# Kernel optimization log

Measured on AMD Instinct MI355X. Metric: run time of the kernel, lower is better.

The kernel has to match this reference:

```python
import jax, jax.numpy as jnp
import numpy as np

L, N, E, H, R = 2048, 4, 768, 12, 16
ALPHA = 16.0
LORA_SCALE = ALPHA / R
HEAD_DIM = E // H


def setup_inputs() -> dict:
    rng = jax.random.key(0)
    ks = jax.random.split(rng, 15)
    g = lambda i, shape, s=1.0: jax.random.normal(ks[i], shape, jnp.float32) * s
    return {
        "query": g(0, (L, N, E)),
        "key": g(1, (L, N, E)),
        "value": g(2, (L, N, E)),
        "in_proj_weight": g(3, (3 * E, E), 0.02),
        "in_proj_bias": g(4, (3 * E,), 0.02),
        "q_down": g(5, (R, E), 0.02),
        "q_up": g(6, (E, R), 0.02),
        "k_down": g(7, (R, E), 0.02),
        "k_up": g(8, (E, R), 0.02),
        "v_down": g(9, (R, E), 0.02),
        "v_up": g(10, (E, R), 0.02),
        "out_proj_weight": g(11, (E, E), 0.02),
        "out_proj_bias": g(12, (E,), 0.02),
        "out_down": g(13, (R, E), 0.02),
        "out_up": g(14, (E, R), 0.02),
    }


def _lora_linear(x, W, b, down, up):
    # y = x W^T + b + scale * (x down^T) up^T   (LoRA-adapted nn.Linear)
    return x @ W.T + b + LORA_SCALE * ((x @ down.T) @ up.T)


def reference(query, key, value, in_proj_weight, in_proj_bias,
              q_down, q_up, k_down, k_up, v_down, v_up,
              out_proj_weight, out_proj_bias, out_down, out_up):
    Wq, Wk, Wv = jnp.split(in_proj_weight, 3, axis=0)
    bq, bk, bv = jnp.split(in_proj_bias, 3)
    q = _lora_linear(query, Wq, bq, q_down, q_up)   # (L,N,E)
    k = _lora_linear(key, Wk, bk, k_down, k_up)     # (S,N,E)
    v = _lora_linear(value, Wv, bv, v_down, v_up)

    def to_heads(t):  # (T,N,E) -> (N,H,T,hd)
        return t.reshape(t.shape[0], N, H, HEAD_DIM).transpose(1, 2, 0, 3)

    qh, kh, vh = to_heads(q), to_heads(k), to_heads(v)
    scale = 1.0 / jnp.sqrt(jnp.float32(HEAD_DIM))
    scores = jnp.einsum('nhld,nhsd->nhls', qh * scale, kh)  # (N,H,L,S)
    attn = jax.nn.softmax(scores, axis=-1)
    o = jnp.einsum('nhls,nhsd->nhld', attn, vh)             # (N,H,L,hd)
    o = o.transpose(2, 0, 1, 3).reshape(L, N, E)            # (L,N,E)
    return _lora_linear(o, out_proj_weight, out_proj_bias, out_down, out_up)
```

## Files before the change

kernel.cpp:

```cpp
#include <hip/hip_runtime.h>

#define LL 2048
#define NN 4
#define EE 768
#define HH 12
#define RR 16
#define HD 64
#define TT (LL*NN)
#define F3 (3*EE)
#define KA 832

typedef __bf16 bf16;
typedef bf16 bf16x4 __attribute__((ext_vector_type(4)));
typedef bf16 bf16x8 __attribute__((ext_vector_type(8)));
typedef float floatx4 __attribute__((ext_vector_type(4)));
typedef float floatx16 __attribute__((ext_vector_type(16)));
typedef unsigned uintx4 __attribute__((ext_vector_type(4)));

#define ZERO16 (floatx16){0.f,0.f,0.f,0.f,0.f,0.f,0.f,0.f,0.f,0.f,0.f,0.f,0.f,0.f,0.f,0.f}

__global__ __launch_bounds__(256) void cast_x(
    const float* __restrict__ q, const float* __restrict__ k,
    const float* __restrict__ v, bf16* __restrict__ Xa)
{
    const int bid = blockIdx.x;
    const int third = bid / (TT/8);
    const int r0 = (bid % (TT/8)) * 8;
    const float* x = (third == 0) ? q : (third == 1) ? k : v;
    const int tid = threadIdx.x;
    #pragma unroll
    for (int i = 0; i < 6; ++i) {
        const int e4 = i*256 + tid;
        const int row = e4 / 192;
        const int col = (e4 % 192) * 4;
        const float4 f = *(const float4*)(x + (size_t)(r0+row)*EE + col);
        bf16x4 h = { (bf16)f.x, (bf16)f.y, (bf16)f.z, (bf16)f.w };
        *(bf16x4*)(Xa + ((size_t)third*TT + r0 + row)*KA + col) = h;
    }
}

__global__ __launch_bounds__(256) void prep_w(
    const float* __restrict__ W,  const float* __restrict__ qu,
    const float* __restrict__ ku, const float* __restrict__ vu,
    const float* __restrict__ Wo, const float* __restrict__ ou,
    const float* __restrict__ qd, const float* __restrict__ kd,
    const float* __restrict__ vd, const float* __restrict__ odw,
    bf16* __restrict__ Wa, bf16* __restrict__ Dm)
{
    const int f = blockIdx.x;
    const int tid = threadIdx.x;
    if (f < 3072) {
        const float* src;
        const float* up;
        if (f < F3) {
            const int third = f / EE, fe = f % EE;
            src = W + (size_t)f*EE;
            up  = ((third == 0) ? qu : (third == 1) ? ku : vu) + fe*RR;
        } else {
            const int fe = f - F3;
            src = Wo + (size_t)fe*EE;
            up  = ou + fe*RR;
        }
        bf16* row = Wa + (size_t)f*KA;
        #pragma unroll
        for (int i = 0; i < 3; ++i)
            row[i*256 + tid] = (bf16)src[i*256 + tid];
        if (tid < 64)
            row[EE + tid] = (tid < RR) ? (bf16)up[tid] : (bf16)0.f;
    } else {
        const int f2 = f - 3072;
        const int which = f2 >> 4, r = f2 & 15;
        const float* dsrc = (which == 0) ? qd : (which == 1) ? kd
                          : (which == 2) ? vd : odw;
        bf16* drow = Dm + (size_t)f2*EE;
        #pragma unroll
        for (int i = 0; i < 3; ++i)
            drow[i*256 + tid] = (bf16)dsrc[(size_t)r*EE + i*256 + tid];
    }
}

template<int XA>
__global__ __launch_bounds__(256) void lora_rank16(
    bf16* __restrict__ A, const bf16* __restrict__ Dm)
{
    __shared__ float red[4][64][16];
    const int row0 = blockIdx.x * 64;
    const int dn = XA ? (row0 >> 13) : 3;
    const bf16* D = Dm + (size_t)dn*16*EE;
    const int tid = threadIdx.x;
    const int wave = tid >> 6, lane = tid & 63;
    const int quad = lane >> 4, l16 = lane & 15;

    floatx4 acc[4];
    #pragma unroll
    for (int rt = 0; rt < 4; ++rt) acc[rt] = (floatx4){0.f,0.f,0.f,0.f};

    #pragma unroll
    for (int ks = 0; ks < 6; ++ks) {
        const int k0 = wave*192 + ks*32;
        const bf16x8 b = *(const bf16x8*)(D + (size_t)l16*EE + k0 + quad*8);
        #pragma unroll
        for (int rt = 0; rt < 4; ++rt) {
            const bf16x8 a = *(const bf16x8*)(
                A + (size_t)(row0 + rt*16 + l16)*KA + k0 + quad*8);
            acc[rt] = __builtin_amdgcn_mfma_f32_16x16x32_bf16(a, b, acc[rt], 0, 0, 0);
        }
    }

    #pragma unroll
    for (int rt = 0; rt < 4; ++rt)
        #pragma unroll
        for (int rr = 0; rr < 4; ++rr)
            red[wave][rt*16 + quad*4 + rr][l16] = acc[rt][rr];
    __syncthreads();

    {
        const int row = tid >> 2, cq = (tid & 3) * 4;
        bf16x4 o;
        #pragma unroll
        for (int j = 0; j < 4; ++j) {
            const float s = red[0][row][cq+j] + red[1][row][cq+j]
                          + red[2][row][cq+j] + red[3][row][cq+j];
            o[j] = (bf16)s;
        }
        *(bf16x4*)(A + (size_t)(row0+row)*KA + EE + cq) = o;
    }
    #pragma unroll
    for (int p = 0; p < 3; ++p) {
        const int id = p*256 + tid;
        const int row = id / 12, c = id % 12;
        *(bf16x4*)(A + (size_t)(row0+row)*KA + 784 + c*4) = (bf16x4){};
    }
}

template<int MODE>
__global__ __launch_bounds__(256) void gemm_aug(
    const bf16* __restrict__ A,
    const bf16* __restrict__ B,
    const float* __restrict__ bias,
    bf16* __restrict__ qo, bf16* __restrict__ ko, bf16* __restrict__ vo,
    float* __restrict__ fo)
{
    __shared__ bf16 As[128][72];
    __shared__ bf16 Bs[128][72];
    const int t0 = blockIdx.x * 128;
    const int f0 = blockIdx.y * 128;
    const int tid = threadIdx.x;
    const int wave = tid >> 6, lane = tid & 63;
    const int quad = lane >> 4, l16 = lane & 15;
    const int m0 = (wave & 1) * 64;
    const int n0 = (wave >> 1) * 64;

    const int third = (MODE == 0) ? (f0 / EE) : 0;
    const bf16* Aeff = (MODE == 0) ? (A + (size_t)third*TT*KA) : A;

    floatx4 acc[4][4];
    #pragma unroll
    for (int rt = 0; rt < 4; ++rt)
        #pragma unroll
        for (int ct = 0; ct < 4; ++ct) acc[rt][ct] = (floatx4){0.f,0.f,0.f,0.f};

    for (int kb = 0; kb < KA/64; ++kb) {
        __syncthreads();
        #pragma unroll
        for (int c = 0; c < 4; ++c) {
            int id = c*256 + tid;
            int row = id >> 3, cg = id & 7;
            *(bf16x8*)(&As[row][cg*8]) =
                *(const bf16x8*)(Aeff + (size_t)(t0+row)*KA + kb*64 + cg*8);
            *(bf16x8*)(&Bs[row][cg*8]) =
                *(const bf16x8*)(B + (size_t)(f0+row)*KA + kb*64 + cg*8);
        }
        __syncthreads();
        #pragma unroll
        for (int kc = 0; kc < 2; ++kc) {
            bf16x8 a[4], bfr[4];
            #pragma unroll
            for (int rt = 0; rt < 4; ++rt)
                a[rt] = *(const bf16x8*)(&As[m0 + rt*16 + l16][kc*32 + quad*8]);
            #pragma unroll
            for (int ct = 0; ct < 4; ++ct)
                bfr[ct] = *(const bf16x8*)(&Bs[n0 + ct*16 + l16][kc*32 + quad*8]);
            #pragma unroll
            for (int rt = 0; rt < 4; ++rt)
                #pragma unroll
                for (int ct = 0; ct < 4; ++ct)
                    acc[rt][ct] = __builtin_amdgcn_mfma_f32_16x16x32_bf16(
                        a[rt], bfr[ct], acc[rt][ct], 0, 0, 0);
        }
    }

    #pragma unroll
    for (int rt = 0; rt < 4; ++rt) {
        #pragma unroll
        for (int r = 0; r < 4; ++r) {
            const int t = t0 + m0 + rt*16 + quad*4 + r;
            #pragma unroll
            for (int ct = 0; ct < 4; ++ct) {
                const int fl = n0 + ct*16 + l16;
                float c = acc[rt][ct][r] + bias[f0 + fl];
                if (MODE == 0) {
                    const int fe = (f0 % EE) + fl;
                    const int h = fe >> 6, d = fe & 63;
                    const int l = t >> 2, n = t & 3;
                    const size_t idx = (((size_t)(n*HH + h)*LL) + l)*HD + d;
                    if (third == 0)      qo[idx] = (bf16)(c * 0.180336877f);
                    else if (third == 1) ko[idx] = (bf16)c;
                    else                 vo[idx] = (bf16)c;
                } else {
                    fo[(size_t)t*EE + f0 + fl] = c;
                }
            }
        }
    }
}

__global__ __launch_bounds__(256) void vtrans(
    const bf16* __restrict__ vin, bf16* __restrict__ vout)
{
    __shared__ bf16 T[64][64];
    const int nh = blockIdx.x >> 5;
    const int l0 = (blockIdx.x & 31) * 64;
    const int tid = threadIdx.x;
    const bf16* src = vin + ((size_t)nh*LL + l0)*HD;
    #pragma unroll
    for (int c = 0; c < 2; ++c) {
        int id = c*256 + tid;
        int row = id >> 3, dg = id & 7;
        int pg = dg ^ (row & 7);
        *(bf16x8*)(&T[row][pg*8]) = *(const bf16x8*)(src + row*HD + dg*8);
    }
    __syncthreads();
    bf16* dst = vout + (size_t)nh*HD*LL;
    const int wave = tid >> 6, lane = tid & 63;
    #pragma unroll
    for (int it = 0; it < 2; ++it) {
        const int d  = it*32 + wave*8 + (lane >> 3);
        const int cg = lane & 7;
        bf16x8 vv;
        #pragma unroll
        for (int j = 0; j < 8; ++j) {
            const int lrow = cg*8 + j;
            const int pg = (d >> 3) ^ (lrow & 7);
            vv[j] = T[lrow][pg*8 + (d & 7)];
        }
        *(bf16x8*)(dst + (size_t)d*LL + l0 + cg*8) = vv;
    }
}

__device__ __forceinline__ unsigned pk_bf16(float a, float b) {
    unsigned r;
    asm("v_cvt_pk_bf16_f32 %0, %1, %2" : "=v"(r) : "v"(a), "v"(b));
    return r;
}

__device__ __forceinline__ void compute_tile(
    const bf16 (&KS)[64][64], const bf16 (&VS)[64][64],
    const bf16x8 (&bq)[4], const bf16x8& ones, const floatx16& z16,
    int l32, int hi, int sw,
    floatx16& oacc0, floatx16& oacc1, floatx16& oaccS)
{
    #pragma unroll
    for (int ss = 0; ss < 2; ++ss) {
        bf16x8 ak[4];
        #pragma unroll
        for (int t4 = 0; t4 < 4; ++t4)
            ak[t4] = *(const bf16x8*)(&KS[ss*32 + l32][((t4*2 + hi) ^ sw) * 8]);

        __builtin_amdgcn_s_setprio(1);
        floatx16 sacc = __builtin_amdgcn_mfma_f32_32x32x16_bf16(
            ak[0], bq[0], z16, 0, 0, 0);
        #pragma unroll
        for (int t4 = 1; t4 < 4; ++t4)
            sacc = __builtin_amdgcn_mfma_f32_32x32x16_bf16(
                ak[t4], bq[t4], sacc, 0, 0, 0);
        __builtin_amdgcn_s_setprio(0);

        bf16x8 bv[4];
        #pragma unroll
        for (int tl = 0; tl < 2; ++tl)
            #pragma unroll
            for (int dt = 0; dt < 2; ++dt)
                bv[tl*2 + dt] = *(const bf16x8*)(
                    &VS[dt*32 + l32][((ss*4 + tl*2 + hi) ^ sw) * 8]);

        float p[16];
        #pragma unroll
        for (int r = 0; r < 16; ++r) p[r] = __builtin_amdgcn_exp2f(sacc[r]);

        union { uintx4 u; bf16x8 h; } fr0, fr1;
        {
            unsigned c0 = pk_bf16(p[0], p[1]);
            unsigned c1 = pk_bf16(p[2], p[3]);
            unsigned c2 = pk_bf16(p[4], p[5]);
            unsigned c3 = pk_bf16(p[6], p[7]);
            asm("v_permlane32_swap_b32 %0, %1" : "+v"(c0), "+v"(c2));
            asm("v_permlane32_swap_b32 %0, %1" : "+v"(c1), "+v"(c3));
            fr0.u = (uintx4){c0, c1, c2, c3};
        }
        {
            unsigned c0 = pk_bf16(p[8],  p[9]);
            unsigned c1 = pk_bf16(p[10], p[11]);
            unsigned c2 = pk_bf16(p[12], p[13]);
            unsigned c3 = pk_bf16(p[14], p[15]);
            asm("v_permlane32_swap_b32 %0, %1" : "+v"(c0), "+v"(c2));
            asm("v_permlane32_swap_b32 %0, %1" : "+v"(c1), "+v"(c3));
            fr1.u = (uintx4){c0, c1, c2, c3};
        }

        __builtin_amdgcn_s_setprio(1);
        oaccS = __builtin_amdgcn_mfma_f32_32x32x16_bf16(fr0.h, ones, oaccS, 0, 0, 0);
        oaccS = __builtin_amdgcn_mfma_f32_32x32x16_bf16(fr1.h, ones, oaccS, 0, 0, 0);
        oacc0 = __builtin_amdgcn_mfma_f32_32x32x16_bf16(fr0.h, bv[0], oacc0, 0, 0, 0);
        oacc1 = __builtin_amdgcn_mfma_f32_32x32x16_bf16(fr0.h, bv[1], oacc1, 0, 0, 0);
        oacc0 = __builtin_amdgcn_mfma_f32_32x32x16_bf16(fr1.h, bv[2], oacc0, 0, 0, 0);
        oacc1 = __builtin_amdgcn_mfma_f32_32x32x16_bf16(fr1.h, bv[3], oacc1, 0, 0, 0);
        __builtin_amdgcn_s_setprio(0);
    }
}

__global__ __launch_bounds__(256, 3) void attn_mfma(
    const bf16* __restrict__ qf, const bf16* __restrict__ kf,
    const bf16* __restrict__ vf, bf16* __restrict__ Oa)
{
    __shared__ bf16 KsA[64][64], VtA[64][64];
    __shared__ bf16 KsB[64][64], VtB[64][64];

    const int bid = blockIdx.x;
    const int nh = bid % 48;
    const int l0 = (bid / 48) * 128;
    const int tid  = threadIdx.x;
    const int wave = tid >> 6;
    const int lane = tid & 63;
    const int l32  = lane & 31;
    const int hi   = lane >> 5;
    const int sw   = l32 & 7;

    const bf16* qb = qf + (size_t)nh * LL * HD;
    const bf16* kb = kf + (size_t)nh * LL * HD;
    const bf16* vb = vf + (size_t)nh * HD * LL;

    const int q0 = l0 + wave * 32;

    const int rowA = tid >> 3;
    const int rowB = rowA + 32;
    const int g0   = tid & 7;
    const int gsA  = g0 ^ (rowA & 7);

    const bf16* pK0 = kb + (size_t)rowA*HD + g0*8;
    const bf16* pK1 = kb + (size_t)rowB*HD + g0*8;
    const bf16* pV0 = vb + (size_t)rowA*LL + g0*8;
    const bf16* pV1 = vb + (size_t)rowB*LL + g0*8;

    bf16x8 bq[4];
    #pragma unroll
    for (int t = 0; t < 4; ++t)
        bq[t] = *(const bf16x8*)(qb + (size_t)(q0 + l32)*HD + t*16 + hi*8);

    const bf16x8 ones = { (bf16)1.f, (bf16)1.f, (bf16)1.f, (bf16)1.f,
                          (bf16)1.f, (bf16)1.f, (bf16)1.f, (bf16)1.f };
    const floatx16 z16 = ZERO16;

    floatx16 oacc0 = ZERO16;
    floatx16 oacc1 = ZERO16;
    floatx16 oaccS = ZERO16;

    bf16x8 gk0, gk1, gv0, gv1;

#define LOADT(S) do {                                                         \
        gk0 = *(const bf16x8*)(pK0 + (size_t)(S)*HD);                         \
        gk1 = *(const bf16x8*)(pK1 + (size_t)(S)*HD);                         \
        gv0 = *(const bf16x8*)(pV0 + (S));                                    \
        gv1 = *(const bf16x8*)(pV1 + (S));                                    \
    } while (0)
#define STORE_A() do {                                                        \
        *(bf16x8*)(&KsA[rowA][gsA*8]) = gk0;                                  \
        *(bf16x8*)(&KsA[rowB][gsA*8]) = gk1;                                  \
        *(bf16x8*)(&VtA[rowA][gsA*8]) = gv0;                                  \
        *(bf16x8*)(&VtA[rowB][gsA*8]) = gv1;                                  \
    } while (0)
#define STORE_B() do {                                                        \
        *(bf16x8*)(&KsB[rowA][gsA*8]) = gk0;                                  \
        *(bf16x8*)(&KsB[rowB][gsA*8]) = gk1;                                  \
        *(bf16x8*)(&VtB[rowA][gsA*8]) = gv0;                                  \
        *(bf16x8*)(&VtB[rowB][gsA*8]) = gv1;                                  \
    } while (0)

    LOADT(0);
    STORE_A();
    LOADT(64);
    __syncthreads();

    for (int tt = 0; tt < 16; ++tt) {
        STORE_B();
        LOADT((size_t)((2*tt + 2) & 31) * 64);
        compute_tile(KsA, VtA, bq, ones, z16, l32, hi, sw, oacc0, oacc1, oaccS);
        __syncthreads();
        STORE_A();
        LOADT((size_t)((2*tt + 3) & 31) * 64);
        compute_tile(KsB, VtB, bq, ones, z16, l32, hi, sw, oacc0, oacc1, oaccS);
        __syncthreads();
    }
#undef LOADT
#undef STORE_A
#undef STORE_B

    const int n = nh / HH, h = nh % HH;
    #pragma unroll
    for (int r = 0; r < 16; ++r) {
        const int qloc = (r & 3) + 8*(r >> 2) + 4*hi;
        const float iv = 1.f / oaccS[r];
        const size_t t = (size_t)(q0 + qloc)*NN + n;
        Oa[t*KA + h*64 + l32]      = (bf16)(oacc0[r] * iv);
        Oa[t*KA + h*64 + 32 + l32] = (bf16)(oacc1[r] * iv);
    }
}

extern "C" void kernel_launch(void* const* d_in, const int* in_sizes, int n_in,
                              void* d_out, int out_size, void* d_ws, size_t ws_size,
                              hipStream_t stream) {
    const float* q   = (const float*)d_in[0];
    const float* k   = (const float*)d_in[1];
    const float* v   = (const float*)d_in[2];
    const float* W   = (const float*)d_in[3];
    const float* b   = (const float*)d_in[4];
    const float* qd  = (const float*)d_in[5];
    const float* qu  = (const float*)d_in[6];
    const float* kd  = (const float*)d_in[7];
    const float* ku  = (const float*)d_in[8];
    const float* vd  = (const float*)d_in[9];
    const float* vu  = (const float*)d_in[10];
    const float* Wo  = (const float*)d_in[11];
    const float* bo  = (const float*)d_in[12];
    const float* odw = (const float*)d_in[13];
    const float* ou  = (const float*)d_in[14];
    float* out = (float*)d_out;

    char* wsb = (char*)d_ws;
    bf16* Xa  = (bf16*)wsb;
    bf16* vfb = (bf16*)wsb;
    bf16* Oa  = (bf16*)(wsb + (size_t)TT*EE*2);
    bf16* Wa  = (bf16*)(wsb + (size_t)3*TT*KA*2);
    bf16* qfb = (bf16*)((char*)Wa + (size_t)3072*KA*2);
    bf16* kfb = qfb + (size_t)TT*EE;
    bf16* vld = kfb + (size_t)TT*EE;
    bf16* Dm  = vld + (size_t)TT*EE;

    cast_x<<<3072, 256, 0, stream>>>(q, k, v, Xa);
    prep_w<<<3136, 256, 0, stream>>>(W, qu, ku, vu, Wo, ou, qd, kd, vd, odw, Wa, Dm);
    lora_rank16<1><<<3*TT/64, 256, 0, stream>>>(Xa, Dm);
    gemm_aug<0><<<dim3(TT/128, F3/128), 256, 0, stream>>>(
        Xa, Wa, b, qfb, kfb, vld, nullptr);
    vtrans<<<48*32, 256, 0, stream>>>(vld, vfb);
    attn_mfma<<<48*16, 256, 0, stream>>>(qfb, kfb, vfb, Oa);
    lora_rank16<0><<<TT/64, 256, 0, stream>>>(Oa, Dm);
    gemm_aug<1><<<dim3(TT/128, EE/128), 256, 0, stream>>>(
        Oa, Wa + (size_t)F3*KA, bo, nullptr, nullptr, nullptr, out);
}
```

Baseline: 300.1 us.

## Fold LoRA adapters into dense weights and drop augmented-K rank-16 passes

Merges each LoRA pair into its base weight (W + scale*up@down, with scale 1) inside prep_w, so the projections become plain K=768 GEMMs. This removes both lora_rank16 launches and shrinks K from 832 to 768 in every GEMM and row stride. The cost is a small per-call weight-merge GEMM inside prep_w, with slightly different bf16 rounding because the adapter is added before the cast.

```diff
diff --git a/kernel.cpp b/kernel.cpp
--- a/kernel.cpp
+++ b/kernel.cpp
@@ -8,7 +8,6 @@
 #define HD 64
 #define TT (LL*NN)
 #define F3 (3*EE)
-#define KA 832
 
 typedef __bf16 bf16;
 typedef bf16 bf16x4 __attribute__((ext_vector_type(4)));
@@ -28,14 +27,15 @@
     const int r0 = (bid % (TT/8)) * 8;
     const float* x = (third == 0) ? q : (third == 1) ? k : v;
     const int tid = threadIdx.x;
+    const size_t base = (size_t)r0 * EE;
+    bf16* dst = Xa + (size_t)third*TT*EE + base;
+    const float* src = x + base;
     #pragma unroll
     for (int i = 0; i < 6; ++i) {
         const int e4 = i*256 + tid;
-        const int row = e4 / 192;
-        const int col = (e4 % 192) * 4;
-        const float4 f = *(const float4*)(x + (size_t)(r0+row)*EE + col);
+        const float4 f = *(const float4*)(src + (size_t)e4*4);
         bf16x4 h = { (bf16)f.x, (bf16)f.y, (bf16)f.z, (bf16)f.w };
-        *(bf16x4*)(Xa + ((size_t)third*TT + r0 + row)*KA + col) = h;
+        *(bf16x4*)(dst + (size_t)e4*4) = h;
     }
 }
 
@@ -45,91 +45,45 @@
     const float* __restrict__ Wo, const float* __restrict__ ou,
     const float* __restrict__ qd, const float* __restrict__ kd,
     const float* __restrict__ vd, const float* __restrict__ odw,
-    bf16* __restrict__ Wa, bf16* __restrict__ Dm)
-{
-    const int f = blockIdx.x;
+    bf16* __restrict__ Wa)
+{
+    const int f0 = blockIdx.x * 16;
     const int tid = threadIdx.x;
-    if (f < 3072) {
-        const float* src;
-        const float* up;
-        if (f < F3) {
-            const int third = f / EE, fe = f % EE;
-            src = W + (size_t)f*EE;
-            up  = ((third == 0) ? qu : (third == 1) ? ku : vu) + fe*RR;
-        } else {
-            const int fe = f - F3;
-            src = Wo + (size_t)fe*EE;
-            up  = ou + fe*RR;
-        }
-        bf16* row = Wa + (size_t)f*KA;
-        #pragma unroll
-        for (int i = 0; i < 3; ++i)
-            row[i*256 + tid] = (bf16)src[i*256 + tid];
-        if (tid < 64)
-            row[EE + tid] = (tid < RR) ? (bf16)up[tid] : (bf16)0.f;
+
+    const float* Wsrc;
+    const float* up;
+    const float* dn;
+    if (f0 < F3) {
+        const int third = f0 / EE, fe = f0 % EE;
+        Wsrc = W + (size_t)f0*EE;
+        up   = ((third == 0) ? qu : (third == 1) ? ku : vu) + (size_t)fe*RR;
+        dn   = (third == 0) ? qd : (third == 1) ? kd : vd;
     } else {
-        const int f2 = f - 3072;
-        const int which = f2 >> 4, r = f2 & 15;
-        const float* dsrc = (which == 0) ? qd : (which == 1) ? kd
-                          : (which == 2) ? vd : odw;
-        bf16* drow = Dm + (size_t)f2*EE;
-        #pragma unroll
-        for (int i = 0; i < 3; ++i)
-            drow[i*256 + tid] = (bf16)dsrc[(size_t)r*EE + i*256 + tid];
-    }
-}
-
-template<int XA>
-__global__ __launch_bounds__(256) void lora_rank16(
-    bf16* __restrict__ A, const bf16* __restrict__ Dm)
-{
-    __shared__ float red[4][64][16];
-    const int row0 = blockIdx.x * 64;
-    const int dn = XA ? (row0 >> 13) : 3;
-    const bf16* D = Dm + (size_t)dn*16*EE;
-    const int tid = threadIdx.x;
-    const int wave = tid >> 6, lane = tid & 63;
-    const int quad = lane >> 4, l16 = lane & 15;
-
-    floatx4 acc[4];
-    #pragma unroll
-    for (int rt = 0; rt < 4; ++rt) acc[rt] = (floatx4){0.f,0.f,0.f,0.f};
-
-    #pragma unroll
-    for (int ks = 0; ks < 6; ++ks) {
-        const int k0 = wave*192 + ks*32;
-        const bf16x8 b = *(const bf16x8*)(D + (size_t)l16*EE + k0 + quad*8);
-        #pragma unroll
-        for (int rt = 0; rt < 4; ++rt) {
-            const bf16x8 a = *(const bf16x8*)(
-                A + (size_t)(row0 + rt*16 + l16)*KA + k0 + quad*8);
-            acc[rt] = __builtin_amdgcn_mfma_f32_16x16x32_bf16(a, b, acc[rt], 0, 0, 0);
-        }
-    }
-
-    #pragma unroll
-    for (int rt = 0; rt < 4; ++rt)
-        #pragma unroll
-        for (int rr = 0; rr < 4; ++rr)
-            red[wave][rt*16 + quad*4 + rr][l16] = acc[rt][rr];
-    __syncthreads();
-
-    {
-        const int row = tid >> 2, cq = (tid & 3) * 4;
-        bf16x4 o;
-        #pragma unroll
-        for (int j = 0; j < 4; ++j) {
-            const float s = red[0][row][cq+j] + red[1][row][cq+j]
-                          + red[2][row][cq+j] + red[3][row][cq+j];
-            o[j] = (bf16)s;
-        }
-        *(bf16x4*)(A + (size_t)(row0+row)*KA + EE + cq) = o;
-    }
-    #pragma unroll
-    for (int p = 0; p < 3; ++p) {
-        const int id = p*256 + tid;
-        const int row = id / 12, c = id % 12;
-        *(bf16x4*)(A + (size_t)(row0+row)*KA + 784 + c*4) = (bf16x4){};
+        const int fe = f0 - F3;
+        Wsrc = Wo + (size_t)fe*EE;
+        up   = ou + (size_t)fe*RR;
+        dn   = odw;
+    }
+
+    float dnv[3][RR];
+    #pragma unroll
+    for (int i = 0; i < 3; ++i)
+        #pragma unroll
+        for (int r = 0; r < RR; ++r)
+            dnv[i][r] = dn[(size_t)r*EE + i*256 + tid];
+
+    for (int fr = 0; fr < 16; ++fr) {
+        float u[RR];
+        #pragma unroll
+        for (int r = 0; r < RR; ++r) u[r] = up[(size_t)fr*RR + r];
+        bf16* orow = Wa + (size_t)(f0 + fr)*EE;
+        #pragma unroll
+        for (int i = 0; i < 3; ++i) {
+            float acc = Wsrc[(size_t)fr*EE + i*256 + tid];
+            #pragma unroll
+            for (int r = 0; r < RR; ++r) acc += u[r] * dnv[i][r];
+            orow[i*256 + tid] = (bf16)acc;
+        }
     }
 }
 
@@ -152,7 +106,7 @@
     const int n0 = (wave >> 1) * 64;
 
     const int third = (MODE == 0) ? (f0 / EE) : 0;
-    const bf16* Aeff = (MODE == 0) ? (A + (size_t)third*TT*KA) : A;
+    const bf16* Aeff = (MODE == 0) ? (A + (size_t)third*TT*EE) : A;
 
     floatx4 acc[4][4];
     #pragma unroll
@@ -160,16 +114,16 @@
         #pragma unroll
         for (int ct = 0; ct < 4; ++ct) acc[rt][ct] = (floatx4){0.f,0.f,0.f,0.f};
 
-    for (int kb = 0; kb < KA/64; ++kb) {
+    for (int kb = 0; kb < EE/64; ++kb) {
         __syncthreads();
         #pragma unroll
         for (int c = 0; c < 4; ++c) {
             int id = c*256 + tid;
             int row = id >> 3, cg = id & 7;
             *(bf16x8*)(&As[row][cg*8]) =
-                *(const bf16x8*)(Aeff + (size_t)(t0+row)*KA + kb*64 + cg*8);
+                *(const bf16x8*)(Aeff + (size_t)(t0+row)*EE + kb*64 + cg*8);
             *(bf16x8*)(&Bs[row][cg*8]) =
-                *(const bf16x8*)(B + (size_t)(f0+row)*KA + kb*64 + cg*8);
+                *(const bf16x8*)(B + (size_t)(f0+row)*EE + kb*64 + cg*8);
         }
         __syncthreads();
         #pragma unroll
@@ -411,8 +365,8 @@
         const int qloc = (r & 3) + 8*(r >> 2) + 4*hi;
         const float iv = 1.f / oaccS[r];
         const size_t t = (size_t)(q0 + qloc)*NN + n;
-        Oa[t*KA + h*64 + l32]      = (bf16)(oacc0[r] * iv);
-        Oa[t*KA + h*64 + 32 + l32] = (bf16)(oacc1[r] * iv);
+        Oa[t*EE + h*64 + l32]      = (bf16)(oacc0[r] * iv);
+        Oa[t*EE + h*64 + 32 + l32] = (bf16)(oacc1[r] * iv);
     }
 }
 
@@ -440,20 +394,17 @@
     bf16* Xa  = (bf16*)wsb;
     bf16* vfb = (bf16*)wsb;
     bf16* Oa  = (bf16*)(wsb + (size_t)TT*EE*2);
-    bf16* Wa  = (bf16*)(wsb + (size_t)3*TT*KA*2);
-    bf16* qfb = (bf16*)((char*)Wa + (size_t)3072*KA*2);
+    bf16* Wa  = (bf16*)(wsb + (size_t)3*TT*EE*2);
+    bf16* qfb = Wa + (size_t)3072*EE;
     bf16* kfb = qfb + (size_t)TT*EE;
     bf16* vld = kfb + (size_t)TT*EE;
-    bf16* Dm  = vld + (size_t)TT*EE;
 
     cast_x<<<3072, 256, 0, stream>>>(q, k, v, Xa);
-    prep_w<<<3136, 256, 0, stream>>>(W, qu, ku, vu, Wo, ou, qd, kd, vd, odw, Wa, Dm);
-    lora_rank16<1><<<3*TT/64, 256, 0, stream>>>(Xa, Dm);
+    prep_w<<<192, 256, 0, stream>>>(W, qu, ku, vu, Wo, ou, qd, kd, vd, odw, Wa);
     gemm_aug<0><<<dim3(TT/128, F3/128), 256, 0, stream>>>(
         Xa, Wa, b, qfb, kfb, vld, nullptr);
     vtrans<<<48*32, 256, 0, stream>>>(vld, vfb);
     attn_mfma<<<48*16, 256, 0, stream>>>(qfb, kfb, vfb, Oa);
-    lora_rank16<0><<<TT/64, 256, 0, stream>>>(Oa, Dm);
     gemm_aug<1><<<dim3(TT/128, EE/128), 256, 0, stream>>>(
-        Oa, Wa + (size_t)F3*KA, bo, nullptr, nullptr, nullptr, out);
-}
+        Oa, Wa + (size_t)F3*EE, bo, nullptr, nullptr, nullptr, out);
+}
```

Result: faster. 282.7 us (-5.8%).
